# Optimization experiments

Hardware: AMD Instinct MI355X
Metric: run time of the kernel (lower is better)

The kernel has to match this reference:

```python
import jax, jax.numpy as jnp
import numpy as np
from jax import lax

B = 1
D, H, W = 16, 16, 32
L = D * H * W
C = 96          # hidden_dim
DIN = 96        # d_inner = expansion_factor(1) * hidden_dim
N = 16          # d_state
R = 6           # dt_rank = ceil(C / 16)
K = 8           # scan directions: 4 axis orders x {fwd, bwd}
PERMS = [(0, 1, 2), (1, 2, 0), (2, 0, 1), (2, 1, 0)]


def _ln(x, w, b, eps):
    m = x.mean(-1, keepdims=True)
    v = ((x - m) ** 2).mean(-1, keepdims=True)
    return (x - m) * lax.rsqrt(v + eps) * w + b


def _conv3d(x, w, b, groups=1):
    y = lax.conv_general_dilated(x, w, (1, 1, 1), 'SAME', feature_group_count=groups,
                                 dimension_numbers=('NCDHW', 'OIDHW', 'NCDHW'))
    return y + b[None, :, None, None, None]


def _ss3d(x5, in_proj_w, conv_w, conv_b, x_proj_w, dt_w, dt_b, A_logs, Ds,
          out_norm_w, out_norm_b, out_proj_w):
    b, d, h, w, _ = x5.shape
    l = d * h * w
    spatial = (d, h, w)
    xz = jnp.einsum('bdhwc,ec->bdhwe', x5, in_proj_w)          # (b,d,h,w,2*DIN)
    x, z = jnp.split(xz, 2, axis=-1)
    x = jnp.transpose(x, (0, 4, 1, 2, 3))                       # (b,DIN,d,h,w)
    x = jax.nn.silu(_conv3d(x, conv_w, conv_b, groups=DIN))     # depthwise conv
    # build K/2 axis-order scans, then add reversed copies -> K directions
    xs = jnp.stack([jnp.transpose(x, (0, 1, 2 + p[0], 2 + p[1], 2 + p[2])).reshape(b, DIN, l)
                    for p in PERMS], axis=1)                    # (b,4,DIN,l)
    xs = jnp.concatenate([xs, jnp.flip(xs, -1)], axis=1)        # (b,K,DIN,l)
    x_dbl = jnp.einsum('bkdl,ked->bkel', xs, x_proj_w)          # e = R+2N
    dts, Bs, Cs = x_dbl[:, :, :R], x_dbl[:, :, R:R + N], x_dbl[:, :, R + N:]
    dts = jax.nn.softplus(jnp.einsum('bkrl,kdr->bkdl', dts, dt_w) + dt_b[None, :, :, None])
    A = -jnp.exp(A_logs)                                        # (K,DIN,N)
    # time-major for the selective scan
    dts_t = jnp.moveaxis(dts, -1, 0)                            # (l,b,K,DIN)
    xs_t = jnp.moveaxis(xs, -1, 0)
    Bs_t = jnp.moveaxis(Bs, -1, 0)                              # (l,b,K,N)
    Cs_t = jnp.moveaxis(Cs, -1, 0)

    def step(hc, inps):
        dt, u, Bt, Ct = inps
        hc = jnp.exp(dt[..., None] * A) * hc + (dt * u)[..., None] * Bt[:, :, None, :]
        y = jnp.einsum('bkdn,bkn->bkd', hc, Ct)
        return hc, y

    h0 = jnp.zeros((b, K, DIN, N), x.dtype)
    _, ys = lax.scan(step, h0, (dts_t, xs_t, Bs_t, Cs_t))       # ys: (l,b,K,DIN)
    ys = jnp.moveaxis(ys, 0, -1) + Ds[None, :, :, None] * xs    # (b,K,DIN,l)
    y_f, y_b = ys[:, :4], jnp.flip(ys[:, 4:], -1)
    acc = jnp.zeros((b, DIN, l), x.dtype)
    for i, p in enumerate(PERMS):
        inv = np.argsort(p)
        pshape = tuple(spatial[ax] for ax in p)
        for yk in (y_f[:, i], y_b[:, i]):
            yk = yk.reshape(b, DIN, *pshape)
            yk = jnp.transpose(yk, (0, 1, 2 + int(inv[0]), 2 + int(inv[1]), 2 + int(inv[2])))
            acc = acc + yk.reshape(b, DIN, l)
    y = _ln(jnp.transpose(acc, (0, 2, 1)), out_norm_w, out_norm_b, 1e-5)
    y = y.reshape(b, d, h, w, DIN) * jax.nn.silu(z)
    return jnp.einsum('bdhwe,ce->bdhwc', y, out_proj_w)


def _cab(x, cab_w1, cab_b1, cab_w2, cab_b2, ca_w1, ca_b1, ca_w2, ca_b2):
    # x: (b,C,d,h,w); conv -> GELU -> conv -> channel attention
    t = jax.nn.gelu(_conv3d(x, cab_w1, cab_b1), approximate=False)
    t = _conv3d(t, cab_w2, cab_b2)
    m = t.mean(axis=(2, 3, 4))                                  # global avg pool (b,C)
    v = jax.nn.relu(m @ ca_w1.T + ca_b1)
    v = jax.nn.sigmoid(v @ ca_w2.T + ca_b2)
    return t * v[:, :, None, None, None]


def _forward(inp, ln1_w, ln1_b, skip1, skip2, ln2_w, ln2_b, in_proj_w, conv_w, conv_b,
             x_proj_w, dt_w, dt_b, A_logs, Ds, out_norm_w, out_norm_b, out_proj_w,
             cab_w1, cab_b1, cab_w2, cab_b2, ca_w1, ca_b1, ca_w2, ca_b2, x_size):
    b, l, c = inp.shape
    d, h, w = x_size
    x5 = inp.reshape(b, d, h, w, c)
    xn = _ln(x5, ln1_w, ln1_b, 1e-6)
    attn = _ss3d(xn, in_proj_w, conv_w, conv_b, x_proj_w, dt_w, dt_b, A_logs, Ds,
                 out_norm_w, out_norm_b, out_proj_w)
    x = x5 * skip1 + attn                                       # drop_path = identity (rate 0)
    y2 = jnp.transpose(_ln(x, ln2_w, ln2_b, 1e-5), (0, 4, 1, 2, 3))
    cab = _cab(y2, cab_w1, cab_b1, cab_w2, cab_b2, ca_w1, ca_b1, ca_w2, ca_b2)
    x = x * skip2 + jnp.transpose(cab, (0, 2, 3, 4, 1))
    return x.reshape(b, l, c)


def setup_inputs() -> dict:
    key = jax.random.key(0)
    ks = jax.random.split(key, 12)
    g = lambda i, shp, s=0.02: jax.random.normal(ks[i], shp, jnp.float32) * s
    return {
        'inp': jax.random.normal(ks[0], (B, L, C), jnp.float32),
        'x_size': (D, H, W),
        'ln1_w': jnp.ones((C,), jnp.float32), 'ln1_b': jnp.zeros((C,), jnp.float32),
        'skip1': jnp.ones((C,), jnp.float32), 'skip2': jnp.ones((C,), jnp.float32),
        'ln2_w': jnp.ones((C,), jnp.float32), 'ln2_b': jnp.zeros((C,), jnp.float32),
        'in_proj_w': g(1, (2 * DIN, C)),
        'conv_w': g(2, (DIN, 1, 3, 3, 3), 0.1), 'conv_b': jnp.zeros((DIN,), jnp.float32),
        'x_proj_w': g(3, (K, R + 2 * N, DIN)),
        'dt_w': g(4, (K, DIN, R), 0.1), 'dt_b': g(5, (K, DIN), 0.1),
        'A_logs': jnp.log(jnp.tile(jnp.arange(1, N + 1, dtype=jnp.float32), (K, DIN, 1))),
        'Ds': jnp.ones((K, DIN), jnp.float32),
        'out_norm_w': jnp.ones((DIN,), jnp.float32), 'out_norm_b': jnp.zeros((DIN,), jnp.float32),
        'out_proj_w': g(6, (C, DIN)),
        'cab_w1': g(7, (C // 3, C, 3, 3, 3), 0.05), 'cab_b1': jnp.zeros((C // 3,), jnp.float32),
        'cab_w2': g(8, (C, C // 3, 3, 3, 3), 0.05), 'cab_b2': jnp.zeros((C,), jnp.float32),
        'ca_w1': g(9, (C // 2, C)), 'ca_b1': jnp.zeros((C // 2,), jnp.float32),
        'ca_w2': g(10, (C, C // 2)), 'ca_b2': jnp.zeros((C,), jnp.float32),
    }


def reference(inp, ln1_w, ln1_b, skip1, skip2, ln2_w, ln2_b, in_proj_w, conv_w, conv_b,
              x_proj_w, dt_w, dt_b, A_logs, Ds, out_norm_w, out_norm_b, out_proj_w,
              cab_w1, cab_b1, cab_w2, cab_b2, ca_w1, ca_b1, ca_w2, ca_b2, x_size):
    return _forward(inp, ln1_w, ln1_b, skip1, skip2, ln2_w, ln2_b, in_proj_w, conv_w, conv_b,
                    x_proj_w, dt_w, dt_b, A_logs, Ds, out_norm_w, out_norm_b, out_proj_w,
                    cab_w1, cab_b1, cab_w2, cab_b2, ca_w1, ca_b1, ca_w2, ca_b2, x_size)
```

## Files before the change

### kernel.cpp

```cpp
#include <hip/hip_runtime.h>
#include <math.h>

#define LL 8192
#define CC 96
#define DINc 96
#define NN 16
#define RR 6
#define KK 8
#define Dd 16
#define Hh 16
#define Ww 32
#define NCH 32
#define CHL 256

__constant__ int Pc_[4][3] = {{0,1,2},{1,2,0},{2,0,1},{2,1,0}};

__device__ __forceinline__ float silu_(float x){ return x / (1.f + __expf(-x)); }

__global__ void k_ln1(const float* __restrict__ inp, const float* __restrict__ w,
                      const float* __restrict__ b, float* __restrict__ xn_cm) {
    int l = blockIdx.x * blockDim.x + threadIdx.x;
    if (l >= LL) return;
    const float* p = inp + l * CC;
    float m = 0.f;
    for (int c = 0; c < CC; ++c) m += p[c];
    m *= (1.f / CC);
    float v = 0.f;
    for (int c = 0; c < CC; ++c) { float d = p[c] - m; v += d * d; }
    v *= (1.f / CC);
    float r = rsqrtf(v + 1e-6f);
    for (int c = 0; c < CC; ++c) xn_cm[c * LL + l] = (p[c] - m) * r * w[c] + b[c];
}

__global__ void k_wtrans(const float* __restrict__ inpj, const float* __restrict__ xpw,
                         const float* __restrict__ w1, const float* __restrict__ w2,
                         const float* __restrict__ opw,
                         float* __restrict__ ipT, float* __restrict__ xpT,
                         float* __restrict__ wT1, float* __restrict__ wT2,
                         float* __restrict__ opT) {
    int idx = blockIdx.x * blockDim.x + threadIdx.x;
    if (idx < 82944) {
        int oc = idx & 31; int tap = (idx >> 5) % 27; int ic = idx / (32 * 27);
        wT1[idx] = w1[(oc * 96 + ic) * 27 + tap];
    }
    if (idx < 82944) {
        int oc = idx % 96; int tap = (idx / 96) % 27; int ic = idx / (96 * 27);
        wT2[idx] = w2[(oc * 32 + ic) * 27 + tap];
    }
    if (idx < 18432) {
        int e = idx % 192; int c = idx / 192;
        ipT[idx] = inpj[e * 96 + c];
    }
    if (idx < 29184) {
        int e = idx % 38; int c = (idx / 38) % 96; int k = idx / (38 * 96);
        xpT[idx] = xpw[(k * 38 + e) * 96 + c];
    }
    if (idx < 9216) {
        int c = idx % 96; int e = idx / 96;
        opT[idx] = opw[c * 96 + e];
    }
}

__global__ void k_inproj(const float* __restrict__ xn_cm, const float* __restrict__ ipT,
                         float* __restrict__ xcm, float* __restrict__ z_rm) {
    int bx = blockIdx.x;
    int eb = bx >> 5;
    int l  = ((bx & 31) << 8) + threadIdx.x;
    int e0 = eb << 3;
    float a[8];
    #pragma unroll
    for (int j = 0; j < 8; ++j) a[j] = 0.f;
    const float* wp = ipT + e0;
    for (int c = 0; c < CC; ++c) {
        float x = xn_cm[c * LL + l];
        const float4* wv = (const float4*)(wp + c * 192);
        float4 wa = wv[0], wb = wv[1];
        a[0] += x * wa.x; a[1] += x * wa.y; a[2] += x * wa.z; a[3] += x * wa.w;
        a[4] += x * wb.x; a[5] += x * wb.y; a[6] += x * wb.z; a[7] += x * wb.w;
    }
    if (e0 < DINc) {
        float* dst = xcm + (long)e0 * LL;
        #pragma unroll
        for (int j = 0; j < 8; ++j) dst[(long)j * LL + l] = a[j];
    } else {
        float* dst = z_rm + (long)l * DINc + (e0 - DINc);
        #pragma unroll
        for (int j = 0; j < 8; ++j) dst[j] = a[j];
    }
}

__global__ void k_dwconv(const float* __restrict__ xcm, const float* __restrict__ cw,
                         const float* __restrict__ cb, float* __restrict__ xs0) {
    int idx = blockIdx.x * blockDim.x + threadIdx.x;
    if (idx >= DINc * LL) return;
    int l = idx & (LL - 1);
    int c = idx >> 13;
    int w = l & (Ww - 1);
    int h = (l >> 5) & (Hh - 1);
    int d = l >> 9;
    float s = cb[c];
    const float* xp = xcm + c * LL;
    const float* wp = cw + c * 27;
    for (int kd = -1; kd <= 1; ++kd) {
        int dd = d + kd; if ((unsigned)dd >= Dd) continue;
        for (int kh = -1; kh <= 1; ++kh) {
            int hh = h + kh; if ((unsigned)hh >= Hh) continue;
            for (int kw = -1; kw <= 1; ++kw) {
                int ww2 = w + kw; if ((unsigned)ww2 >= Ww) continue;
                s += xp[(dd * Hh + hh) * Ww + ww2] * wp[(kd + 1) * 9 + (kh + 1) * 3 + (kw + 1)];
            }
        }
    }
    xs0[c * LL + l] = silu_(s);
}

__global__ void k_permA(float* __restrict__ xs) {
    int idx = blockIdx.x * blockDim.x + threadIdx.x;
    if (idx >= 3 * DINc * LL) return;
    int l = idx & (LL - 1);
    int c = (idx >> 13) % DINc;
    int k = idx / (DINc * LL) + 1;
    int p0 = Pc_[k][0], p1 = Pc_[k][1], p2 = Pc_[k][2];
    const int sp[3] = {Dd, Hh, Ww};
    int pd1 = sp[p1], pd2 = sp[p2];
    int i2 = l % pd2;
    int t  = l / pd2;
    int i1 = t % pd1;
    int i0 = t / pd1;
    int coord[3];
    coord[p0] = i0; coord[p1] = i1; coord[p2] = i2;
    int o = (coord[0] * Hh + coord[1]) * Ww + coord[2];
    xs[(k * DINc + c) * LL + l] = xs[c * LL + o];
}

__global__ void k_permB(float* __restrict__ xs) {
    int idx = blockIdx.x * blockDim.x + threadIdx.x;
    if (idx >= 4 * DINc * LL) return;
    int l = idx & (LL - 1);
    int c = (idx >> 13) % DINc;
    int k = idx / (DINc * LL);
    xs[((long)(k + 4) * DINc + c) * LL + l] = xs[((long)k * DINc + c) * LL + (LL - 1 - l)];
}

__global__ void k_xdbl(const float* __restrict__ xs, const float* __restrict__ xpT,
                       float* __restrict__ dtr, float* __restrict__ Bb, float* __restrict__ Cb) {
    int bx = blockIdx.x;
    int k = bx >> 5;
    int l = ((bx & 31) << 8) + threadIdx.x;
    float acc[38];
    #pragma unroll
    for (int e = 0; e < 38; ++e) acc[e] = 0.f;
    const float* xb = xs + (long)k * DINc * LL + l;
    const float* wb = xpT + k * DINc * 38;
    for (int c = 0; c < DINc; ++c) {
        float x = xb[(long)c * LL];
        const float* wr = wb + c * 38;
        #pragma unroll
        for (int e = 0; e < 38; ++e) acc[e] += x * wr[e];
    }
    float* dtp = dtr + ((long)k * LL + l) * 6;
    #pragma unroll
    for (int r = 0; r < RR; ++r) dtp[r] = acc[r];
    int lq = l >> 2, q = l & 3;
    float* Bp = Bb + (((long)k * 2048 + lq) * 16) * 4 + q;
    float* Cp = Cb + (((long)k * 2048 + lq) * 16) * 4 + q;
    #pragma unroll
    for (int n = 0; n < NN; ++n) { Bp[n * 4] = acc[RR + n]; Cp[n * 4] = acc[RR + NN + n]; }
}

__device__ __forceinline__ float softplus_(float x) {
    return (x > 20.f) ? x : __logf(1.f + __expf(x));
}

__global__ __launch_bounds__(512)
void k_scanf(float* __restrict__ xs_ys, const float* __restrict__ dtr,
             const float* __restrict__ Bb, const float* __restrict__ Cb,
             const float* __restrict__ A_logs, const float* __restrict__ dt_w,
             const float* __restrict__ dt_b, const float* __restrict__ Ds) {
    __shared__ __align__(16) float sdt[LL + (LL >> 7) * 4];
    __shared__ float sAp[16][33];
    __shared__ float sBc[16][33];
    __shared__ float shs[16][33];
    int bx = blockIdx.x;
    int grp = (bx & 7) * DINc + (bx >> 3);
    int k = grp / DINc;
    int tid = threadIdx.x;
    int n = tid & 15;
    int chunk = tid >> 4;
    {
        float w0 = dt_w[grp * RR + 0], w1 = dt_w[grp * RR + 1], w2 = dt_w[grp * RR + 2];
        float w3 = dt_w[grp * RR + 3], w4 = dt_w[grp * RR + 4], w5 = dt_w[grp * RR + 5];
        float dtb = dt_b[grp];
        const float* drb = dtr + (long)k * LL * 6;
        for (int i = tid; i < LL; i += 512) {
            const float2* dp = (const float2*)(drb + (long)i * 6);
            float2 d0 = dp[0], d1 = dp[1], d2 = dp[2];
            float dtl = dtb + d0.x * w0 + d0.y * w1 + d1.x * w2 + d1.y * w3 + d2.x * w4 + d2.y * w5;
            sdt[i + ((i >> 7) << 2)] = softplus_(dtl);
        }
    }
    __syncthreads();
    float A_n = -__expf(A_logs[grp * NN + n]);
    const float4* sdt4 = (const float4*)sdt;
    int dbase = chunk * 66;
    const float4* u4 = (const float4*)(xs_ys + (long)grp * LL + chunk * CHL);
    const float4* B4 = (const float4*)Bb + ((long)k * 2048 + chunk * (CHL / 4)) * 16 + n;
    const float4* C4 = (const float4*)Cb + ((long)k * 2048 + chunk * (CHL / 4)) * 16 + n;
    {
        float hc = 0.f, dsum = 0.f;
        #pragma unroll 4
        for (int q = 0; q < CHL / 4; ++q) {
            float4 dt = sdt4[dbase + q + (q >> 5)];
            float4 uu = u4[q];
            float4 Bv = B4[q * 16];
            dsum += (dt.x + dt.y) + (dt.z + dt.w);
            hc = __expf(dt.x * A_n) * hc + (dt.x * uu.x) * Bv.x;
            hc = __expf(dt.y * A_n) * hc + (dt.y * uu.y) * Bv.y;
            hc = __expf(dt.z * A_n) * hc + (dt.z * uu.z) * Bv.z;
            hc = __expf(dt.w * A_n) * hc + (dt.w * uu.w) * Bv.w;
        }
        sAp[n][chunk] = __expf(A_n * dsum);
        sBc[n][chunk] = hc;
    }
    __syncthreads();
    if (tid < 16) {
        float h = 0.f;
        for (int c = 0; c < NCH; ++c) {
            shs[tid][c] = h;
            h = sAp[tid][c] * h + sBc[tid][c];
        }
    }
    __syncthreads();
    float Dv = Ds[grp];
    float* urow = xs_ys + (long)grp * LL + chunk * CHL;
    float hc = shs[n][chunk];
    int qsel = n >> 2, csel = n & 3;
    bool b0 = (n & 1), b1 = ((n >> 1) & 1), b2 = ((n >> 2) & 1), b3 = (n >> 3);
    for (int base = 0; base < CHL; base += 16) {
        float u_lane = 0.f;
        float p[16];
        #pragma unroll
        for (int q = 0; q < 4; ++q) {
            int qq = (base >> 2) + q;
            float4 dt = sdt4[dbase + qq + (qq >> 5)];
            float4 uu = *(const float4*)(urow + base + q * 4);
            float4 Bv = B4[qq * 16];
            float4 Cv = C4[qq * 16];
            if (q == qsel)
                u_lane = (csel == 0) ? uu.x : (csel == 1) ? uu.y : (csel == 2) ? uu.z : uu.w;
            hc = __expf(dt.x * A_n) * hc + (dt.x * uu.x) * Bv.x;  p[q*4+0] = hc * Cv.x;
            hc = __expf(dt.y * A_n) * hc + (dt.y * uu.y) * Bv.y;  p[q*4+1] = hc * Cv.y;
            hc = __expf(dt.z * A_n) * hc + (dt.z * uu.z) * Bv.z;  p[q*4+2] = hc * Cv.z;
            hc = __expf(dt.w * A_n) * hc + (dt.w * uu.w) * Bv.w;  p[q*4+3] = hc * Cv.w;
        }
        float q8[8];
        #pragma unroll
        for (int m = 0; m < 8; ++m) {
            float sel = b0 ? p[2*m] : p[2*m+1];
            float r = __shfl_xor(sel, 1, 16);
            q8[m] = (b0 ? p[2*m+1] : p[2*m]) + r;
        }
        float r4[4];
        #pragma unroll
        for (int m = 0; m < 4; ++m) {
            float sel = b1 ? q8[2*m] : q8[2*m+1];
            float r = __shfl_xor(sel, 2, 16);
            r4[m] = (b1 ? q8[2*m+1] : q8[2*m]) + r;
        }
        float t2r[2];
        #pragma unroll
        for (int m = 0; m < 2; ++m) {
            float sel = b2 ? r4[2*m] : r4[2*m+1];
            float r = __shfl_xor(sel, 4, 16);
            t2r[m] = (b2 ? r4[2*m+1] : r4[2*m]) + r;
        }
        float sel = b3 ? t2r[0] : t2r[1];
        float r = __shfl_xor(sel, 8, 16);
        float yv = (b3 ? t2r[1] : t2r[0]) + r;
        urow[base + n] = yv + Dv * u_lane;
    }
}

__global__ void k_combproj(const float* __restrict__ ys, const float* __restrict__ z_rm,
                           const float* __restrict__ w, const float* __restrict__ b,
                           const float* __restrict__ opT, const float* __restrict__ inp,
                           const float* __restrict__ skip1, float* __restrict__ xafter) {
    __shared__ float sy[4][96];
    int wave = threadIdx.x >> 6;
    int lane = threadIdx.x & 63;
    int l = blockIdx.x * 4 + wave;
    int d = l >> 9, h = (l >> 5) & 15, wd = l & 31;
    int lps[4];
    lps[0] = l;
    lps[1] = (h * 32 + wd) * 16 + d;
    lps[2] = (wd * 16 + d) * 16 + h;
    lps[3] = (wd * 16 + h) * 16 + d;
    int c0 = lane, c1 = 64 + lane;
    float a0 = 0.f, a1 = 0.f;
    #pragma unroll
    for (int i = 0; i < 4; ++i) {
        a0 += ys[((long)(i * 96) + c0) * LL + lps[i]];
        a0 += ys[((long)((4 + i) * 96) + c0) * LL + (LL - 1 - lps[i])];
    }
    if (lane < 32) {
        #pragma unroll
        for (int i = 0; i < 4; ++i) {
            a1 += ys[((long)(i * 96) + c1) * LL + lps[i]];
            a1 += ys[((long)((4 + i) * 96) + c1) * LL + (LL - 1 - lps[i])];
        }
    }
    float s = a0 + a1;
    #pragma unroll
    for (int o = 1; o < 64; o <<= 1) s += __shfl_xor(s, o, 64);
    float m = s * (1.f / 96.f);
    float d0 = a0 - m;
    float d1 = (lane < 32) ? (a1 - m) : 0.f;
    float ss = d0 * d0 + d1 * d1;
    #pragma unroll
    for (int o = 1; o < 64; o <<= 1) ss += __shfl_xor(ss, o, 64);
    float r = rsqrtf(ss * (1.f / 96.f) + 1e-5f);
    float zz = z_rm[(long)l * 96 + c0];
    sy[wave][c0] = (d0 * r * w[c0] + b[c0]) * silu_(zz);
    if (lane < 32) {
        float z1 = z_rm[(long)l * 96 + c1];
        sy[wave][c1] = (d1 * r * w[c1] + b[c1]) * silu_(z1);
    }
    __syncthreads();
    int c1g = (lane < 32) ? c1 : 0;
    float o0 = 0.f, o1 = 0.f;
    #pragma unroll 4
    for (int e = 0; e < 96; ++e) {
        float ye = sy[wave][e];
        o0 += ye * opT[e * 96 + c0];
        o1 += ye * opT[e * 96 + c1g];
    }
    xafter[(long)l * 96 + c0] = inp[(long)l * 96 + c0] * skip1[c0] + o0;
    if (lane < 32)
        xafter[(long)l * 96 + c1] = inp[(long)l * 96 + c1] * skip1[c1] + o1;
}

__global__ void k_ln2(const float* __restrict__ xafter, const float* __restrict__ w,
                      const float* __restrict__ b, float* __restrict__ y2) {
    int l = blockIdx.x * blockDim.x + threadIdx.x;
    if (l >= LL) return;
    const float* p = xafter + l * CC;
    float m = 0.f;
    for (int c = 0; c < CC; ++c) m += p[c];
    m *= (1.f / CC);
    float v = 0.f;
    for (int c = 0; c < CC; ++c) { float d = p[c] - m; v += d * d; }
    v *= (1.f / CC);
    float r = rsqrtf(v + 1e-5f);
    for (int c = 0; c < CC; ++c) y2[c * LL + l] = (p[c] - m) * r * w[c] + b[c];
}

__global__ void k_conv1(const float* __restrict__ y2, const float* __restrict__ wT,
                        float* __restrict__ part) {
    int bx = blockIdx.x;
    int g  = bx >> 3;
    int ocg = g & 3;
    int isp = g >> 2;
    int l4 = ((bx & 7) << 8) + threadIdx.x;
    int w0 = (l4 & 7) << 2;
    int h  = (l4 >> 3) & 15;
    int d  = l4 >> 7;
    int l  = (d * Hh + h) * Ww + w0;
    float rmask[9]; int roff[9];
    #pragma unroll
    for (int kd = 0; kd < 3; ++kd) {
        int dd = d + kd - 1;
        bool vd = (unsigned)dd < Dd; int dc = vd ? dd : 0;
        #pragma unroll
        for (int kh = 0; kh < 3; ++kh) {
            int hh = h + kh - 1;
            bool vh = (unsigned)hh < Hh; int hcl = vh ? hh : 0;
            rmask[kd * 3 + kh] = (vd && vh) ? 1.f : 0.f;
            roff[kd * 3 + kh]  = (dc * Hh + hcl) * Ww + w0;
        }
    }
    float mleft  = (w0 > 0)  ? 1.f : 0.f;
    float mright = (w0 < 28) ? 1.f : 0.f;
    float acc[32];
    #pragma unroll
    for (int j = 0; j < 32; ++j) acc[j] = 0.f;
    for (int ic = isp * 6; ic < isp * 6 + 6; ++ic) {
        const float* xp = y2 + (long)ic * LL;
        const float* wb = wT + ic * 864 + ocg * 8;
        #pragma unroll
        for (int r = 0; r < 9; ++r) {
            float rm = rmask[r];
            const float* xr = xp + roff[r];
            float4 xc = *(const float4*)xr;
            float v[6];
            v[0] = xr[-1] * (rm * mleft);
            v[1] = xc.x * rm; v[2] = xc.y * rm; v[3] = xc.z * rm; v[4] = xc.w * rm;
            v[5] = xr[4] * (rm * mright);
            #pragma unroll
            for (int t = 0; t < 3; ++t) {
                const float4* wv = (const float4*)(wb + (r * 3 + t) * 32);
                float4 wa = wv[0], wbv = wv[1];
                #pragma unroll
                for (int p = 0; p < 4; ++p) {
                    float x = v[t + p];
                    acc[0  + p] += x * wa.x;  acc[4  + p] += x * wa.y;
                    acc[8  + p] += x * wa.z;  acc[12 + p] += x * wa.w;
                    acc[16 + p] += x * wbv.x; acc[20 + p] += x * wbv.y;
                    acc[24 + p] += x * wbv.z; acc[28 + p] += x * wbv.w;
                }
            }
        }
    }
    float* pp = part + ((long)(isp * 32 + ocg * 8)) * LL + l;
    #pragma unroll
    for (int oc = 0; oc < 8; ++oc)
        *(float4*)(pp + (long)oc * LL) = make_float4(acc[oc*4+0], acc[oc*4+1], acc[oc*4+2], acc[oc*4+3]);
}

__global__ void k_gelusum(const float* __restrict__ part, const float* __restrict__ b1,
                          float* __restrict__ t1) {
    int idx = blockIdx.x * blockDim.x + threadIdx.x;
    if (idx >= 32 * LL) return;
    int l = idx & (LL - 1);
    int oc = idx >> 13;
    float s = b1[oc];
    #pragma unroll
    for (int isp = 0; isp < 16; ++isp)
        s += part[((long)(isp * 32 + oc)) * LL + l];
    t1[oc * LL + l] = 0.5f * s * (1.f + erff(s * 0.70710678118654752f));
}

__global__ void k_conv2(const float* __restrict__ t1, const float* __restrict__ wT,
                        float* __restrict__ part) {
    int bx = blockIdx.x;
    int g  = bx >> 3;
    int ocg = g % 12;
    int isp = g / 12;
    int l4 = ((bx & 7) << 8) + threadIdx.x;
    int w0 = (l4 & 7) << 2;
    int h  = (l4 >> 3) & 15;
    int d  = l4 >> 7;
    int l  = (d * Hh + h) * Ww + w0;
    float rmask[9]; int roff[9];
    #pragma unroll
    for (int kd = 0; kd < 3; ++kd) {
        int dd = d + kd - 1;
        bool vd = (unsigned)dd < Dd; int dc = vd ? dd : 0;
        #pragma unroll
        for (int kh = 0; kh < 3; ++kh) {
            int hh = h + kh - 1;
            bool vh = (unsigned)hh < Hh; int hcl = vh ? hh : 0;
            rmask[kd * 3 + kh] = (vd && vh) ? 1.f : 0.f;
            roff[kd * 3 + kh]  = (dc * Hh + hcl) * Ww + w0;
        }
    }
    float mleft  = (w0 > 0)  ? 1.f : 0.f;
    float mright = (w0 < 28) ? 1.f : 0.f;
    float acc[32];
    #pragma unroll
    for (int j = 0; j < 32; ++j) acc[j] = 0.f;
    for (int ic = isp * 4; ic < isp * 4 + 4; ++ic) {
        const float* xp = t1 + (long)ic * LL;
        const float* wb = wT + ic * 2592 + ocg * 8;
        #pragma unroll
        for (int r = 0; r < 9; ++r) {
            float rm = rmask[r];
            const float* xr = xp + roff[r];
            float4 xc = *(const float4*)xr;
            float v[6];
            v[0] = xr[-1] * (rm * mleft);
            v[1] = xc.x * rm; v[2] = xc.y * rm; v[3] = xc.z * rm; v[4] = xc.w * rm;
            v[5] = xr[4] * (rm * mright);
            #pragma unroll
            for (int t = 0; t < 3; ++t) {
                const float4* wv = (const float4*)(wb + (r * 3 + t) * 96);
                float4 wa = wv[0], wbv = wv[1];
                #pragma unroll
                for (int p = 0; p < 4; ++p) {
                    float x = v[t + p];
                    acc[0  + p] += x * wa.x;  acc[4  + p] += x * wa.y;
                    acc[8  + p] += x * wa.z;  acc[12 + p] += x * wa.w;
                    acc[16 + p] += x * wbv.x; acc[20 + p] += x * wbv.y;
                    acc[24 + p] += x * wbv.z; acc[28 + p] += x * wbv.w;
                }
            }
        }
    }
    float* pp = part + ((long)(isp * 96 + ocg * 8)) * LL + l;
    #pragma unroll
    for (int oc = 0; oc < 8; ++oc)
        *(float4*)(pp + (long)oc * LL) = make_float4(acc[oc*4+0], acc[oc*4+1], acc[oc*4+2], acc[oc*4+3]);
}

__global__ void k_conv2sum(const float* __restrict__ part, const float* __restrict__ b2,
                           float* __restrict__ t2) {
    int idx = blockIdx.x * blockDim.x + threadIdx.x;
    if (idx >= 96 * LL) return;
    int l = idx & (LL - 1);
    int oc = idx >> 13;
    float s = b2[oc];
    #pragma unroll
    for (int isp = 0; isp < 8; ++isp)
        s += part[((long)(isp * 96 + oc)) * LL + l];
    t2[oc * LL + l] = s;
}

__global__ void k_mean(const float* __restrict__ t2, float* __restrict__ mbuf) {
    __shared__ float sm[256];
    int c = blockIdx.x;
    const float4* tp = (const float4*)(t2 + (long)c * LL);
    float a = 0.f;
    for (int q = threadIdx.x; q < LL / 4; q += 256) {
        float4 v = tp[q];
        a += (v.x + v.y) + (v.z + v.w);
    }
    sm[threadIdx.x] = a;
    __syncthreads();
    for (int o = 128; o > 0; o >>= 1) {
        if (threadIdx.x < o) sm[threadIdx.x] += sm[threadIdx.x + o];
        __syncthreads();
    }
    if (threadIdx.x == 0) mbuf[c] = sm[0] * (1.f / LL);
}

__global__ void k_mlp(const float* __restrict__ mbuf, const float* __restrict__ w1,
                      const float* __restrict__ b1, const float* __restrict__ w2,
                      const float* __restrict__ b2, float* __restrict__ v2) {
    __shared__ float v[48];
    int t = threadIdx.x;
    if (t < 48) {
        float s = b1[t];
        for (int c = 0; c < 96; ++c) s += mbuf[c] * w1[t * 96 + c];
        v[t] = fmaxf(s, 0.f);
    }
    __syncthreads();
    if (t < 96) {
        float s = b2[t];
        for (int j = 0; j < 48; ++j) s += v[j] * w2[t * 48 + j];
        v2[t] = 1.f / (1.f + __expf(-s));
    }
}

__global__ void k_final(const float* __restrict__ xafter, const float* __restrict__ skip2,
                        const float* __restrict__ t2, const float* __restrict__ v2,
                        float* __restrict__ out) {
    __shared__ float tile[96][17];
    __shared__ float sk2[96], sv2[96];
    int l0 = blockIdx.x * 16;
    int tid = threadIdx.x;
    if (tid < 96) { sk2[tid] = skip2[tid]; sv2[tid] = v2[tid]; }
    #pragma unroll
    for (int r = 0; r < 6; ++r) {
        int e = r * 256 + tid;
        int c = e >> 4, lo = e & 15;
        tile[c][lo] = t2[(long)c * LL + l0 + lo];
    }
    __syncthreads();
    #pragma unroll
    for (int r = 0; r < 6; ++r) {
        int e = r * 256 + tid;
        int lo = e / 96, c = e % 96;
        long gi = (long)(l0 + lo) * 96 + c;
        out[gi] = xafter[gi] * sk2[c] + tile[c][lo] * sv2[c];
    }
}

static const size_t OFF_XS     = 0;
static const size_t OFF_Z      = 6291456;
static const size_t OFF_XCM    = 7077888;
static const size_t OFF_XN     = 7864320;
static const size_t OFF_DTRAW  = 8650752;
static const size_t OFF_BB     = 9043968;
static const size_t OFF_CB     = 10092544;
static const size_t OFF_XAFTER = 11141120;
static const size_t OFF_Y2     = 11927552;
static const size_t OFF_T1     = 12713984;
static const size_t OFF_T2     = 12976128;
static const size_t OFF_MV     = 13762560;
static const size_t OFF_WT1    = 13762816;
static const size_t OFF_WT2    = 13845760;
static const size_t OFF_IPT    = 13928704;
static const size_t OFF_XPT    = 13947136;
static const size_t OFF_OPT    = 13976320;

extern "C" void kernel_launch(void* const* d_in, const int* in_sizes, int n_in,
                              void* d_out, int out_size, void* d_ws, size_t ws_size,
                              hipStream_t stream) {
    const float* inp    = (const float*)d_in[0];
    const float* ln1_w  = (const float*)d_in[2];
    const float* ln1_b  = (const float*)d_in[3];
    const float* skip1  = (const float*)d_in[4];
    const float* skip2  = (const float*)d_in[5];
    const float* ln2_w  = (const float*)d_in[6];
    const float* ln2_b  = (const float*)d_in[7];
    const float* inpj   = (const float*)d_in[8];
    const float* conv_w = (const float*)d_in[9];
    const float* conv_b = (const float*)d_in[10];
    const float* xpw    = (const float*)d_in[11];
    const float* dt_w   = (const float*)d_in[12];
    const float* dt_b   = (const float*)d_in[13];
    const float* A_logs = (const float*)d_in[14];
    const float* Ds     = (const float*)d_in[15];
    const float* onw    = (const float*)d_in[16];
    const float* onb    = (const float*)d_in[17];
    const float* opw    = (const float*)d_in[18];
    const float* cab_w1 = (const float*)d_in[19];
    const float* cab_b1 = (const float*)d_in[20];
    const float* cab_w2 = (const float*)d_in[21];
    const float* cab_b2 = (const float*)d_in[22];
    const float* ca_w1  = (const float*)d_in[23];
    const float* ca_b1  = (const float*)d_in[24];
    const float* ca_w2  = (const float*)d_in[25];
    const float* ca_b2  = (const float*)d_in[26];

    float* ws = (float*)d_ws;
    float* xs     = ws + OFF_XS;
    float* zbuf   = ws + OFF_Z;
    float* xcm    = ws + OFF_XCM;
    float* xn     = ws + OFF_XN;
    float* dtr    = ws + OFF_DTRAW;
    float* Bb     = ws + OFF_BB;
    float* Cb     = ws + OFF_CB;
    float* xafter = ws + OFF_XAFTER;
    float* y2     = ws + OFF_Y2;
    float* t1     = ws + OFF_T1;
    float* t2     = ws + OFF_T2;
    float* mv     = ws + OFF_MV;
    float* wT1    = ws + OFF_WT1;
    float* wT2    = ws + OFF_WT2;
    float* ipT    = ws + OFF_IPT;
    float* xpT    = ws + OFF_XPT;
    float* opT    = ws + OFF_OPT;
    float* part1  = xs;
    float* part2  = xs;

    float* out = (float*)d_out;
    #define GRID(n) dim3((unsigned)(((n) + 255) / 256)), dim3(256)

    hipLaunchKernelGGL(k_ln1,     GRID(LL),                   0, stream, inp, ln1_w, ln1_b, xn);
    hipLaunchKernelGGL(k_wtrans,  GRID(82944),                0, stream, inpj, xpw, cab_w1, cab_w2, opw, ipT, xpT, wT1, wT2, opT);
    hipLaunchKernelGGL(k_inproj,  dim3(768), dim3(256),       0, stream, xn, ipT, xcm, zbuf);
    hipLaunchKernelGGL(k_dwconv,  GRID(DINc * LL),            0, stream, xcm, conv_w, conv_b, xs);
    hipLaunchKernelGGL(k_permA,   GRID(3 * DINc * LL),        0, stream, xs);
    hipLaunchKernelGGL(k_permB,   GRID(4 * DINc * LL),        0, stream, xs);
    hipLaunchKernelGGL(k_xdbl,    dim3(256), dim3(256),       0, stream, xs, xpT, dtr, Bb, Cb);
    hipLaunchKernelGGL(k_scanf,   dim3(KK * DINc), dim3(512), 0, stream, xs, dtr, Bb, Cb, A_logs, dt_w, dt_b, Ds);
    hipLaunchKernelGGL(k_combproj,dim3(LL / 4), dim3(256),    0, stream, xs, zbuf, onw, onb, opT, inp, skip1, xafter);
    hipLaunchKernelGGL(k_ln2,     GRID(LL),                   0, stream, xafter, ln2_w, ln2_b, y2);
    hipLaunchKernelGGL(k_conv1,   dim3(512), dim3(256),       0, stream, y2, wT1, part1);
    hipLaunchKernelGGL(k_gelusum, GRID(32 * LL),              0, stream, part1, cab_b1, t1);
    hipLaunchKernelGGL(k_conv2,   dim3(768), dim3(256),       0, stream, t1, wT2, part2);
    hipLaunchKernelGGL(k_conv2sum,GRID(96 * LL),              0, stream, part2, cab_b2, t2);
    hipLaunchKernelGGL(k_mean,    dim3(96), dim3(256),        0, stream, t2, mv);
    hipLaunchKernelGGL(k_mlp,     dim3(1), dim3(128),         0, stream, mv, ca_w1, ca_b1, ca_w2, ca_b2, mv + 96);
    hipLaunchKernelGGL(k_final,   dim3(512), dim3(256),       0, stream, xafter, skip2, t2, mv + 96, out);
    #undef GRID
}
```

Before: 326.4 us.

## Vectorize depthwise conv and flip copy, tile LN2 through shared memory

The depthwise 3D conv now computes four outputs per thread from float4 row loads, with the weights held in registers and masks replacing branches. The reverse-copy kernel moves float4 elements and reverses them within each vector. LN2 stages a 16-token tile in shared memory, computes mean and variance with sub-wave shuffles, and writes the channel-major output coalesced instead of strided per thread. The aim is fewer memory transactions and better coalescing in small bandwidth-bound kernels, at the cost of more complex indexing and reads of clamped, masked neighbours.

```diff
diff --git a/kernel.cpp b/kernel.cpp
--- a/kernel.cpp
+++ b/kernel.cpp
@@ -91,27 +91,52 @@
 
 __global__ void k_dwconv(const float* __restrict__ xcm, const float* __restrict__ cw,
                          const float* __restrict__ cb, float* __restrict__ xs0) {
-    int idx = blockIdx.x * blockDim.x + threadIdx.x;
-    if (idx >= DINc * LL) return;
-    int l = idx & (LL - 1);
-    int c = idx >> 13;
-    int w = l & (Ww - 1);
-    int h = (l >> 5) & (Hh - 1);
-    int d = l >> 9;
-    float s = cb[c];
-    const float* xp = xcm + c * LL;
-    const float* wp = cw + c * 27;
-    for (int kd = -1; kd <= 1; ++kd) {
-        int dd = d + kd; if ((unsigned)dd >= Dd) continue;
-        for (int kh = -1; kh <= 1; ++kh) {
-            int hh = h + kh; if ((unsigned)hh >= Hh) continue;
-            for (int kw = -1; kw <= 1; ++kw) {
-                int ww2 = w + kw; if ((unsigned)ww2 >= Ww) continue;
-                s += xp[(dd * Hh + hh) * Ww + ww2] * wp[(kd + 1) * 9 + (kh + 1) * 3 + (kw + 1)];
-            }
-        }
-    }
-    xs0[c * LL + l] = silu_(s);
+    int bx = blockIdx.x;
+    int c  = bx >> 3;
+    int l4 = ((bx & 7) << 8) + threadIdx.x;
+    int w0 = (l4 & 7) << 2;
+    int h  = (l4 >> 3) & 15;
+    int d  = l4 >> 7;
+    int l  = (d * Hh + h) * Ww + w0;
+    float wk[27];
+    #pragma unroll
+    for (int t = 0; t < 27; ++t) wk[t] = cw[c * 27 + t];
+    float rmask[9]; int roff[9];
+    #pragma unroll
+    for (int kd = 0; kd < 3; ++kd) {
+        int dd = d + kd - 1;
+        bool vd = (unsigned)dd < Dd; int dc = vd ? dd : 0;
+        #pragma unroll
+        for (int kh = 0; kh < 3; ++kh) {
+            int hh = h + kh - 1;
+            bool vh = (unsigned)hh < Hh; int hcl = vh ? hh : 0;
+            rmask[kd * 3 + kh] = (vd && vh) ? 1.f : 0.f;
+            roff[kd * 3 + kh]  = (dc * Hh + hcl) * Ww + w0;
+        }
+    }
+    float mleft  = (w0 > 0)  ? 1.f : 0.f;
+    float mright = (w0 < 28) ? 1.f : 0.f;
+    float a0 = cb[c], a1 = a0, a2 = a0, a3 = a0;
+    const float* xp = xcm + (long)c * LL;
+    #pragma unroll
+    for (int r = 0; r < 9; ++r) {
+        float rm = rmask[r];
+        const float* xr = xp + roff[r];
+        float4 xc = *(const float4*)xr;
+        float v[6];
+        v[0] = xr[-1] * (rm * mleft);
+        v[1] = xc.x * rm; v[2] = xc.y * rm; v[3] = xc.z * rm; v[4] = xc.w * rm;
+        v[5] = xr[4] * (rm * mright);
+        #pragma unroll
+        for (int t = 0; t < 3; ++t) {
+            float wv = wk[r * 3 + t];
+            a0 += v[t + 0] * wv;
+            a1 += v[t + 1] * wv;
+            a2 += v[t + 2] * wv;
+            a3 += v[t + 3] * wv;
+        }
+    }
+    *(float4*)(xs0 + (long)c * LL + l) = make_float4(silu_(a0), silu_(a1), silu_(a2), silu_(a3));
 }
 
 __global__ void k_permA(float* __restrict__ xs) {
@@ -135,11 +160,14 @@
 
 __global__ void k_permB(float* __restrict__ xs) {
     int idx = blockIdx.x * blockDim.x + threadIdx.x;
-    if (idx >= 4 * DINc * LL) return;
-    int l = idx & (LL - 1);
-    int c = (idx >> 13) % DINc;
-    int k = idx / (DINc * LL);
-    xs[((long)(k + 4) * DINc + c) * LL + l] = xs[((long)k * DINc + c) * LL + (LL - 1 - l)];
+    if (idx >= 4 * DINc * (LL / 4)) return;
+    int q = idx & (LL / 4 - 1);
+    int c = (idx >> 11) % DINc;
+    int k = idx / (DINc * (LL / 4));
+    const float4* src = (const float4*)(xs + ((long)k * DINc + c) * LL);
+    float4 s = src[LL / 4 - 1 - q];
+    float4* dst = (float4*)(xs + ((long)(k + 4) * DINc + c) * LL);
+    dst[q] = make_float4(s.w, s.z, s.y, s.x);
 }
 
 __global__ void k_xdbl(const float* __restrict__ xs, const float* __restrict__ xpT,
@@ -341,17 +369,39 @@
 
 __global__ void k_ln2(const float* __restrict__ xafter, const float* __restrict__ w,
                       const float* __restrict__ b, float* __restrict__ y2) {
-    int l = blockIdx.x * blockDim.x + threadIdx.x;
-    if (l >= LL) return;
-    const float* p = xafter + l * CC;
-    float m = 0.f;
-    for (int c = 0; c < CC; ++c) m += p[c];
-    m *= (1.f / CC);
-    float v = 0.f;
-    for (int c = 0; c < CC; ++c) { float d = p[c] - m; v += d * d; }
-    v *= (1.f / CC);
-    float r = rsqrtf(v + 1e-5f);
-    for (int c = 0; c < CC; ++c) y2[c * LL + l] = (p[c] - m) * r * w[c] + b[c];
+    __shared__ float tile[16][97];
+    __shared__ float smean[16], srstd[16];
+    int l0 = blockIdx.x * 16;
+    int tid = threadIdx.x;
+    #pragma unroll
+    for (int r = 0; r < 6; ++r) {
+        int e = r * 256 + tid;
+        int lo = e / 96, c = e % 96;
+        tile[lo][c] = xafter[(long)(l0 + lo) * 96 + c];
+    }
+    __syncthreads();
+    {
+        int lo = tid >> 4, g = tid & 15;
+        float ps = 0.f;
+        #pragma unroll
+        for (int j = 0; j < 6; ++j) ps += tile[lo][g * 6 + j];
+        #pragma unroll
+        for (int o = 1; o < 16; o <<= 1) ps += __shfl_xor(ps, o, 16);
+        float m = ps * (1.f / 96.f);
+        float pv = 0.f;
+        #pragma unroll
+        for (int j = 0; j < 6; ++j) { float dd = tile[lo][g * 6 + j] - m; pv += dd * dd; }
+        #pragma unroll
+        for (int o = 1; o < 16; o <<= 1) pv += __shfl_xor(pv, o, 16);
+        if (g == 0) { smean[lo] = m; srstd[lo] = rsqrtf(pv * (1.f / 96.f) + 1e-5f); }
+    }
+    __syncthreads();
+    #pragma unroll
+    for (int r = 0; r < 6; ++r) {
+        int e = r * 256 + tid;
+        int c = e >> 4, lo = e & 15;
+        y2[(long)c * LL + l0 + lo] = (tile[lo][c] - smean[lo]) * srstd[lo] * w[c] + b[c];
+    }
 }
 
 __global__ void k_conv1(const float* __restrict__ y2, const float* __restrict__ wT,
@@ -639,13 +689,13 @@
     hipLaunchKernelGGL(k_ln1,     GRID(LL),                   0, stream, inp, ln1_w, ln1_b, xn);
     hipLaunchKernelGGL(k_wtrans,  GRID(82944),                0, stream, inpj, xpw, cab_w1, cab_w2, opw, ipT, xpT, wT1, wT2, opT);
     hipLaunchKernelGGL(k_inproj,  dim3(768), dim3(256),       0, stream, xn, ipT, xcm, zbuf);
-    hipLaunchKernelGGL(k_dwconv,  GRID(DINc * LL),            0, stream, xcm, conv_w, conv_b, xs);
+    hipLaunchKernelGGL(k_dwconv,  dim3(768), dim3(256),       0, stream, xcm, conv_w, conv_b, xs);
     hipLaunchKernelGGL(k_permA,   GRID(3 * DINc * LL),        0, stream, xs);
-    hipLaunchKernelGGL(k_permB,   GRID(4 * DINc * LL),        0, stream, xs);
+    hipLaunchKernelGGL(k_permB,   GRID(4 * DINc * (LL / 4)),  0, stream, xs);
     hipLaunchKernelGGL(k_xdbl,    dim3(256), dim3(256),       0, stream, xs, xpT, dtr, Bb, Cb);
     hipLaunchKernelGGL(k_scanf,   dim3(KK * DINc), dim3(512), 0, stream, xs, dtr, Bb, Cb, A_logs, dt_w, dt_b, Ds);
     hipLaunchKernelGGL(k_combproj,dim3(LL / 4), dim3(256),    0, stream, xs, zbuf, onw, onb, opT, inp, skip1, xafter);
-    hipLaunchKernelGGL(k_ln2,     GRID(LL),                   0, stream, xafter, ln2_w, ln2_b, y2);
+    hipLaunchKernelGGL(k_ln2,     dim3(512), dim3(256),       0, stream, xafter, ln2_w, ln2_b, y2);
     hipLaunchKernelGGL(k_conv1,   dim3(512), dim3(256),       0, stream, y2, wT1, part1);
     hipLaunchKernelGGL(k_gelusum, GRID(32 * LL),              0, stream, part1, cab_b1, t1);
     hipLaunchKernelGGL(k_conv2,   dim3(768), dim3(256),       0, stream, t1, wT2, part2);
```

Result: faster. 306.7 us (-6.0%).
